# Optimization experiments

Measured on AMD Instinct MI355X. Metric: run time of the kernel, lower is better.

The kernel has to match this reference:

```python
import jax, jax.numpy as jnp
import numpy as np

INF = 10000.0
HEAD_SIZE = 64
HEADS = 12


def _rope_tables(seqlen, dim, dtype=jnp.float32):
    inv_freq = 1.0 / (10000.0 ** (jnp.arange(0, dim, 2, dtype=dtype) / dim))
    t = jnp.arange(seqlen, dtype=dtype)
    freqs = t[:, None] * inv_freq[None, :]  # [n, dim//2]
    return jnp.sin(freqs), jnp.cos(freqs)


def _apply_rope(t, sin, cos):
    # t: [b, n, d]; sin/cos: [n, d//2]
    t1, t2 = t[..., 0::2], t[..., 1::2]
    r1 = t1 * cos - t2 * sin
    r2 = t1 * sin + t2 * cos
    return jnp.stack([r1, r2], axis=-1).reshape(t.shape)


def setup_inputs() -> dict:
    key = jax.random.key(0)
    k1, k2, k3, k4, k5, k6 = jax.random.split(key, 6)
    B, N, H = 16, 512, 1024
    inputs = jax.random.normal(k1, (B, N, H), dtype=jnp.float32)
    attention_mask = jax.random.randint(k2, (B, N), 0, 2, dtype=jnp.int32)
    w1 = jax.random.normal(k3, (H, 2 * HEAD_SIZE), dtype=jnp.float32) * 0.02
    b1 = jax.random.normal(k4, (2 * HEAD_SIZE,), dtype=jnp.float32) * 0.02
    w2 = jax.random.normal(k5, (2 * HEAD_SIZE, 2 * HEADS), dtype=jnp.float32) * 0.02
    b2 = jax.random.normal(k6, (2 * HEADS,), dtype=jnp.float32) * 0.02
    return {"inputs": inputs, "attention_mask": attention_mask,
            "w1": w1, "b1": b1, "w2": w2, "b2": b2}


def reference(inputs, attention_mask, w1, b1, w2, b2):
    B, N, _ = inputs.shape
    x = inputs @ w1 + b1  # [b, n, 2*head_size]
    qw, kw = x[..., 0::2], x[..., 1::2]  # each [b, n, head_size]
    sin, cos = _rope_tables(N, HEAD_SIZE, x.dtype)
    qw = _apply_rope(qw, sin, cos)
    kw = _apply_rope(kw, sin, cos)
    logits = jnp.einsum('bmd,bnd->bmn', qw, kw) / (HEAD_SIZE ** 0.5)
    bias = jnp.swapaxes(x @ w2 + b2, 1, 2) / 2.0  # [b, 2*heads, n]
    logits = logits[:, None] + bias[:, 0::2, None, :] + bias[:, 1::2, :, None]  # [b, h, m, n]
    am = attention_mask.astype(logits.dtype)
    pad_mask = 1.0 - am[:, None, None, :] * am[:, None, :, None]
    logits = logits - pad_mask * INF
    idx = jnp.arange(N)
    tril = (idx[:, None] > idx[None, :]).astype(logits.dtype)  # strict lower triangle
    logits = logits - tril * INF
    return logits
```

## Files before the change

kernel.cpp:

```cpp
#include <hip/hip_runtime.h>

typedef __bf16 bf16_t;
typedef bf16_t bf16x4 __attribute__((ext_vector_type(4)));
typedef bf16_t bf16x8 __attribute__((ext_vector_type(8)));
typedef float f32x4 __attribute__((ext_vector_type(4)));

#define INFV 10000.0f

__global__ __launch_bounds__(256) void k0_transpose(const float* __restrict__ w1,
                                                    bf16_t* __restrict__ w1T) {
    __shared__ float s[32][36];
    const int t = threadIdx.x;
    const int k0 = (blockIdx.x & 31) * 32;
    const int c0 = (blockIdx.x >> 5) * 32;
    {
        const int r = t >> 3, cc = (t & 7) * 4;
        *(float4*)&s[r][cc] = *(const float4*)&w1[(size_t)(k0 + r) * 128 + c0 + cc];
    }
    __syncthreads();
    {
        const int cr = t >> 3, kk = (t & 7) * 4;
        bf16x4 v;
        v[0] = (bf16_t)s[kk + 0][cr];
        v[1] = (bf16_t)s[kk + 1][cr];
        v[2] = (bf16_t)s[kk + 2][cr];
        v[3] = (bf16_t)s[kk + 3][cr];
        *(bf16x4*)&w1T[(size_t)(c0 + cr) * 1024 + k0 + kk] = v;
    }
}

__global__ __launch_bounds__(512) void k1_proj(
    const float* __restrict__ inputs,
    const bf16_t* __restrict__ w1T,
    const float* __restrict__ b1,
    const float* __restrict__ w2,
    const float* __restrict__ b2,
    bf16_t* __restrict__ qg,
    bf16_t* __restrict__ kg,
    float* __restrict__ biasT)
{
    __shared__ bf16_t s_a[2][32][72];
    __shared__ float s_x[32][132];
    __shared__ float s_w2T[24][132];

    const int t = threadIdx.x;
    const int row0 = blockIdx.x * 32;
    const int lane = t & 63, wave = t >> 6;
    const int cn = lane & 15, kgrp = lane >> 4;
    const int rg = (wave & 1) * 16;
    const int cg = (wave >> 1) * 32;

    for (int i = t; i < 3072; i += 512) {
        int j = i / 24, c = i - j * 24;
        s_w2T[c][j] = w2[i];
    }

    const int sr = t >> 4;
    const int sc = (t & 15) * 4;
    const float* asrc = inputs + (size_t)(row0 + sr) * 1024 + sc;

    const bf16_t* bp0 = w1T + (size_t)(cg + 0 * 16 + cn) * 1024 + kgrp * 8;
    const bf16_t* bp1 = w1T + (size_t)(cg + 1 * 16 + cn) * 1024 + kgrp * 8;

    f32x4 acc[2][2] = {};
    float4 pfA[2];
    bf16x8 bfr[2][2][2];

    {
        float4 v = *(const float4*)(asrc);
        bf16x4 b;
        b[0] = (bf16_t)v.x; b[1] = (bf16_t)v.y; b[2] = (bf16_t)v.z; b[3] = (bf16_t)v.w;
        *(bf16x4*)&s_a[0][sr][sc] = b;
    }
    pfA[1] = *(const float4*)(asrc + 64);
    pfA[0] = *(const float4*)(asrc + 128);
    bfr[0][0][0] = *(const bf16x8*)(bp0 + 0);
    bfr[0][0][1] = *(const bf16x8*)(bp0 + 32);
    bfr[0][1][0] = *(const bf16x8*)(bp1 + 0);
    bfr[0][1][1] = *(const bf16x8*)(bp1 + 32);
    __syncthreads();

#pragma unroll
    for (int kt = 0; kt < 16; ++kt) {
        const int p = kt & 1;
        if (kt < 15) {
            const int o = (kt + 1) * 64;
            bfr[p ^ 1][0][0] = *(const bf16x8*)(bp0 + o);
            bfr[p ^ 1][0][1] = *(const bf16x8*)(bp0 + o + 32);
            bfr[p ^ 1][1][0] = *(const bf16x8*)(bp1 + o);
            bfr[p ^ 1][1][1] = *(const bf16x8*)(bp1 + o + 32);
        }
        {
            bf16x8 af0 = *(const bf16x8*)&s_a[p][rg + cn][kgrp * 8];
            bf16x8 af1 = *(const bf16x8*)&s_a[p][rg + cn][32 + kgrp * 8];
            acc[0][p] = __builtin_amdgcn_mfma_f32_16x16x32_bf16(af0, bfr[p][0][0], acc[0][p], 0, 0, 0);
            acc[0][p] = __builtin_amdgcn_mfma_f32_16x16x32_bf16(af1, bfr[p][0][1], acc[0][p], 0, 0, 0);
            acc[1][p] = __builtin_amdgcn_mfma_f32_16x16x32_bf16(af0, bfr[p][1][0], acc[1][p], 0, 0, 0);
            acc[1][p] = __builtin_amdgcn_mfma_f32_16x16x32_bf16(af1, bfr[p][1][1], acc[1][p], 0, 0, 0);
        }
        if (kt < 15) {
            float4 v = pfA[(kt + 1) & 1];
            bf16x4 b;
            b[0] = (bf16_t)v.x; b[1] = (bf16_t)v.y; b[2] = (bf16_t)v.z; b[3] = (bf16_t)v.w;
            *(bf16x4*)&s_a[p ^ 1][sr][sc] = b;
        }
        if (kt < 13) {
            pfA[(kt + 3) & 1] = *(const float4*)(asrc + (kt + 3) * 64);
        }
        __syncthreads();
    }

#pragma unroll
    for (int tt = 0; tt < 2; ++tt) {
        const int col = cg + tt * 16 + cn;
        const float bb = b1[col];
        f32x4 sum = acc[tt][0] + acc[tt][1];
#pragma unroll
        for (int r = 0; r < 4; ++r)
            s_x[rg + kgrp * 4 + r][col] = sum[r] + bb;
    }
    __syncthreads();

    {
        const int r = t >> 4;
        const int i0 = (t & 15) * 2;
        const int rowg = row0 + r;
        const int n = rowg & 511;
        bf16x4 qv, kv;
#pragma unroll
        for (int u = 0; u < 2; ++u) {
            const int i = i0 + u;
            float fr = (float)n * exp2f((float)i * -0.4152410118609203f);
            float sv, cv;
            sincosf(fr, &sv, &cv);
            float x0 = s_x[r][4 * i + 0];
            float x1 = s_x[r][4 * i + 1];
            float x2 = s_x[r][4 * i + 2];
            float x3 = s_x[r][4 * i + 3];
            qv[2 * u]     = (bf16_t)(x0 * cv - x2 * sv);
            qv[2 * u + 1] = (bf16_t)(x0 * sv + x2 * cv);
            kv[2 * u]     = (bf16_t)(x1 * cv - x3 * sv);
            kv[2 * u + 1] = (bf16_t)(x1 * sv + x3 * cv);
        }
        *(bf16x4*)&qg[(size_t)rowg * 64 + 2 * i0] = qv;
        *(bf16x4*)&kg[(size_t)rowg * 64 + 2 * i0] = kv;
    }

    {
        const int r = t >> 4;
        const int cb = t & 15;
        if (cb < 12) {
            const int c0 = cb * 2;
            float sum0 = 0.f, sum1 = 0.f;
#pragma unroll 4
            for (int j = 0; j < 128; j += 4) {
                float4 xv = *(const float4*)&s_x[r][j];
                float4 wa = *(const float4*)&s_w2T[c0 + 0][j];
                float4 wb = *(const float4*)&s_w2T[c0 + 1][j];
                sum0 += xv.x * wa.x + xv.y * wa.y + xv.z * wa.z + xv.w * wa.w;
                sum1 += xv.x * wb.x + xv.y * wb.y + xv.z * wb.z + xv.w * wb.w;
            }
            const int rowg = row0 + r;
            const int bb = rowg >> 9, n = rowg & 511;
            float* bp = biasT + (size_t)bb * 12288 + n;
            bp[(size_t)(c0 + 0) * 512] = (sum0 + b2[c0 + 0]) * 0.5f;
            bp[(size_t)(c0 + 1) * 512] = (sum1 + b2[c0 + 1]) * 0.5f;
        }
    }
}

__global__ __launch_bounds__(256) void k2_logits(
    const bf16_t* __restrict__ qg, const bf16_t* __restrict__ kg,
    const float* __restrict__ biasT, const int* __restrict__ am,
    float* __restrict__ out)
{
    __shared__ float s_be[12][64], s_bo[12][64];
    __shared__ float s_pm[64], s_pn[64];

    const int t = threadIdx.x;
    const int b = blockIdx.z;
    const int m0 = blockIdx.y * 64;
    const int n0 = blockIdx.x * 64;

    for (int i = t; i < 768; i += 256) {
        const int h = i >> 6, j = i & 63;
        s_be[h][j] = biasT[(size_t)b * 12288 + (size_t)(2 * h) * 512 + n0 + j];
        s_bo[h][j] = biasT[(size_t)b * 12288 + (size_t)(2 * h + 1) * 512 + m0 + j];
    }
    if (t < 64) s_pm[t] = (float)am[b * 512 + m0 + t];
    else if (t < 128) s_pn[t - 64] = (float)am[b * 512 + n0 + (t - 64)];

    const int lane = t & 63, wave = t >> 6;
    const int cn = lane & 15, kgrp = lane >> 4;

    const bf16_t* qp = qg + ((size_t)(b * 512 + m0 + wave * 16 + cn)) * 64 + kgrp * 8;
    bf16x8 qb0 = *(const bf16x8*)qp;
    bf16x8 qb1 = *(const bf16x8*)(qp + 32);

    f32x4 acc[4] = {};
#pragma unroll
    for (int nt = 0; nt < 4; ++nt) {
        const bf16_t* kp = kg + ((size_t)(b * 512 + n0 + nt * 16 + cn)) * 64 + kgrp * 8;
        bf16x8 ka0 = *(const bf16x8*)kp;
        bf16x8 ka1 = *(const bf16x8*)(kp + 32);
        acc[nt] = __builtin_amdgcn_mfma_f32_16x16x32_bf16(ka0, qb0, acc[nt], 0, 0, 0);
        acc[nt] = __builtin_amdgcn_mfma_f32_16x16x32_bf16(ka1, qb1, acc[nt], 0, 0, 0);
    }
    __syncthreads();

    const int rgrp = lane >> 4;
    const int m_loc = wave * 16 + cn;
    const int m = m0 + m_loc;
    const float am_m = s_pm[m_loc];

#pragma unroll
    for (int nt = 0; nt < 4; ++nt) {
#pragma unroll
        for (int r = 0; r < 4; ++r) {
            const int n_loc = nt * 16 + rgrp * 4 + r;
            float v = acc[nt][r] * 0.125f;
            v -= (1.0f - am_m * s_pn[n_loc]) * INFV;
            if (m > n0 + n_loc) v -= INFV;
            acc[nt][r] = v;
        }
    }

    float* ob = out + (size_t)b * 3145728 + (size_t)m * 512 + n0;
#pragma unroll
    for (int h = 0; h < 12; ++h) {
        const float bo = s_bo[h][m_loc];
        const f32x4 bov = {bo, bo, bo, bo};
#pragma unroll
        for (int nt = 0; nt < 4; ++nt) {
            const f32x4 be4 = *(const f32x4*)&s_be[h][nt * 16 + rgrp * 4];
            f32x4 w = acc[nt] + be4 + bov;
            *(f32x4*)&ob[(size_t)h * 262144 + nt * 16 + rgrp * 4] = w;
        }
    }
}

extern "C" void kernel_launch(void* const* d_in, const int* in_sizes, int n_in,
                              void* d_out, int out_size, void* d_ws, size_t ws_size,
                              hipStream_t stream) {
    const float* inputs = (const float*)d_in[0];
    const int*   am     = (const int*)d_in[1];
    const float* w1     = (const float*)d_in[2];
    const float* b1     = (const float*)d_in[3];
    const float* w2     = (const float*)d_in[4];
    const float* b2     = (const float*)d_in[5];
    float* out = (float*)d_out;

    bf16_t* w1T   = (bf16_t*)d_ws;
    bf16_t* qg    = w1T + 131072;
    bf16_t* kg    = qg + 524288;
    float*  biasT = (float*)(kg + 524288);

    k0_transpose<<<128, 256, 0, stream>>>(w1, w1T);
    k1_proj<<<256, 512, 0, stream>>>(inputs, w1T, b1, w2, b2, qg, kg, biasT);
    k2_logits<<<dim3(8, 8, 16), 256, 0, stream>>>(qg, kg, biasT, am, out);
}
```

Measured before the change: 67.16 us.

## Fuse projection and logits kernels with a global atomic grid barrier

Merges the projection kernel and the logits kernel into one persistent launch of 256 blocks. A global atomic counter acts as a grid-wide barrier once Q, K and the bias are written. After the barrier each 512-thread block splits into two 256-thread halves, and each half handles two 64x64 logits tiles. This removes one kernel launch and the gap between kernels, but relies on all 256 blocks being co-resident and adds a memset plus spin-waiting. The logits phase also runs with fewer resident blocks than the previous 1024-block grid, which may lower the overlap of memory traffic on the write-bound output.

```diff
diff --git a/kernel.cpp b/kernel.cpp
--- a/kernel.cpp
+++ b/kernel.cpp
@@ -29,212 +29,229 @@
     }
 }
 
-__global__ __launch_bounds__(512) void k1_proj(
+__global__ __launch_bounds__(512) void k12_fused(
     const float* __restrict__ inputs,
     const bf16_t* __restrict__ w1T,
     const float* __restrict__ b1,
     const float* __restrict__ w2,
     const float* __restrict__ b2,
+    const int* __restrict__ am,
     bf16_t* __restrict__ qg,
     bf16_t* __restrict__ kg,
-    float* __restrict__ biasT)
+    float* __restrict__ biasT,
+    float* __restrict__ out,
+    unsigned* __restrict__ ctr)
 {
     __shared__ bf16_t s_a[2][32][72];
     __shared__ float s_x[32][132];
     __shared__ float s_w2T[24][132];
+    __shared__ float s_be[2][12][64], s_bo[2][12][64];
+    __shared__ float s_pm[2][64], s_pn[2][64];
 
     const int t = threadIdx.x;
-    const int row0 = blockIdx.x * 32;
-    const int lane = t & 63, wave = t >> 6;
-    const int cn = lane & 15, kgrp = lane >> 4;
-    const int rg = (wave & 1) * 16;
-    const int cg = (wave >> 1) * 32;
-
-    for (int i = t; i < 3072; i += 512) {
-        int j = i / 24, c = i - j * 24;
-        s_w2T[c][j] = w2[i];
-    }
-
-    const int sr = t >> 4;
-    const int sc = (t & 15) * 4;
-    const float* asrc = inputs + (size_t)(row0 + sr) * 1024 + sc;
-
-    const bf16_t* bp0 = w1T + (size_t)(cg + 0 * 16 + cn) * 1024 + kgrp * 8;
-    const bf16_t* bp1 = w1T + (size_t)(cg + 1 * 16 + cn) * 1024 + kgrp * 8;
-
-    f32x4 acc[2][2] = {};
-    float4 pfA[2];
-    bf16x8 bfr[2][2][2];
-
-    {
-        float4 v = *(const float4*)(asrc);
-        bf16x4 b;
-        b[0] = (bf16_t)v.x; b[1] = (bf16_t)v.y; b[2] = (bf16_t)v.z; b[3] = (bf16_t)v.w;
-        *(bf16x4*)&s_a[0][sr][sc] = b;
-    }
-    pfA[1] = *(const float4*)(asrc + 64);
-    pfA[0] = *(const float4*)(asrc + 128);
-    bfr[0][0][0] = *(const bf16x8*)(bp0 + 0);
-    bfr[0][0][1] = *(const bf16x8*)(bp0 + 32);
-    bfr[0][1][0] = *(const bf16x8*)(bp1 + 0);
-    bfr[0][1][1] = *(const bf16x8*)(bp1 + 32);
-    __syncthreads();
-
-#pragma unroll
-    for (int kt = 0; kt < 16; ++kt) {
-        const int p = kt & 1;
-        if (kt < 15) {
-            const int o = (kt + 1) * 64;
-            bfr[p ^ 1][0][0] = *(const bf16x8*)(bp0 + o);
-            bfr[p ^ 1][0][1] = *(const bf16x8*)(bp0 + o + 32);
-            bfr[p ^ 1][1][0] = *(const bf16x8*)(bp1 + o);
-            bfr[p ^ 1][1][1] = *(const bf16x8*)(bp1 + o + 32);
-        }
+
+    {
+        const int row0 = blockIdx.x * 32;
+        const int lane = t & 63, wave = t >> 6;
+        const int cn = lane & 15, kgrp = lane >> 4;
+        const int rg = (wave & 1) * 16;
+        const int cg = (wave >> 1) * 32;
+
+        for (int i = t; i < 3072; i += 512) {
+            int j = i / 24, c = i - j * 24;
+            s_w2T[c][j] = w2[i];
+        }
+
+        const int sr = t >> 4;
+        const int sc = (t & 15) * 4;
+        const float* asrc = inputs + (size_t)(row0 + sr) * 1024 + sc;
+
+        const bf16_t* bp0 = w1T + (size_t)(cg + 0 * 16 + cn) * 1024 + kgrp * 8;
+        const bf16_t* bp1 = w1T + (size_t)(cg + 1 * 16 + cn) * 1024 + kgrp * 8;
+
+        f32x4 acc[2][2] = {};
+        float4 pfA[2];
+        bf16x8 bfr[2][2][2];
+
         {
-            bf16x8 af0 = *(const bf16x8*)&s_a[p][rg + cn][kgrp * 8];
-            bf16x8 af1 = *(const bf16x8*)&s_a[p][rg + cn][32 + kgrp * 8];
-            acc[0][p] = __builtin_amdgcn_mfma_f32_16x16x32_bf16(af0, bfr[p][0][0], acc[0][p], 0, 0, 0);
-            acc[0][p] = __builtin_amdgcn_mfma_f32_16x16x32_bf16(af1, bfr[p][0][1], acc[0][p], 0, 0, 0);
-            acc[1][p] = __builtin_amdgcn_mfma_f32_16x16x32_bf16(af0, bfr[p][1][0], acc[1][p], 0, 0, 0);
-            acc[1][p] = __builtin_amdgcn_mfma_f32_16x16x32_bf16(af1, bfr[p][1][1], acc[1][p], 0, 0, 0);
-        }
-        if (kt < 15) {
-            float4 v = pfA[(kt + 1) & 1];
+            float4 v = *(const float4*)(asrc);
             bf16x4 b;
             b[0] = (bf16_t)v.x; b[1] = (bf16_t)v.y; b[2] = (bf16_t)v.z; b[3] = (bf16_t)v.w;
-            *(bf16x4*)&s_a[p ^ 1][sr][sc] = b;
-        }
-        if (kt < 13) {
-            pfA[(kt + 3) & 1] = *(const float4*)(asrc + (kt + 3) * 64);
-        }
+            *(bf16x4*)&s_a[0][sr][sc] = b;
+        }
+        pfA[1] = *(const float4*)(asrc + 64);
+        pfA[0] = *(const float4*)(asrc + 128);
+        bfr[0][0][0] = *(const bf16x8*)(bp0 + 0);
+        bfr[0][0][1] = *(const bf16x8*)(bp0 + 32);
+        bfr[0][1][0] = *(const bf16x8*)(bp1 + 0);
+        bfr[0][1][1] = *(const bf16x8*)(bp1 + 32);
         __syncthreads();
-    }
-
-#pragma unroll
-    for (int tt = 0; tt < 2; ++tt) {
-        const int col = cg + tt * 16 + cn;
-        const float bb = b1[col];
-        f32x4 sum = acc[tt][0] + acc[tt][1];
-#pragma unroll
-        for (int r = 0; r < 4; ++r)
-            s_x[rg + kgrp * 4 + r][col] = sum[r] + bb;
-    }
+
+#pragma unroll
+        for (int kt = 0; kt < 16; ++kt) {
+            const int p = kt & 1;
+            if (kt < 15) {
+                const int o = (kt + 1) * 64;
+                bfr[p ^ 1][0][0] = *(const bf16x8*)(bp0 + o);
+                bfr[p ^ 1][0][1] = *(const bf16x8*)(bp0 + o + 32);
+                bfr[p ^ 1][1][0] = *(const bf16x8*)(bp1 + o);
+                bfr[p ^ 1][1][1] = *(const bf16x8*)(bp1 + o + 32);
+            }
+            {
+                bf16x8 af0 = *(const bf16x8*)&s_a[p][rg + cn][kgrp * 8];
+                bf16x8 af1 = *(const bf16x8*)&s_a[p][rg + cn][32 + kgrp * 8];
+                acc[0][p] = __builtin_amdgcn_mfma_f32_16x16x32_bf16(af0, bfr[p][0][0], acc[0][p], 0, 0, 0);
+                acc[0][p] = __builtin_amdgcn_mfma_f32_16x16x32_bf16(af1, bfr[p][0][1], acc[0][p], 0, 0, 0);
+                acc[1][p] = __builtin_amdgcn_mfma_f32_16x16x32_bf16(af0, bfr[p][1][0], acc[1][p], 0, 0, 0);
+                acc[1][p] = __builtin_amdgcn_mfma_f32_16x16x32_bf16(af1, bfr[p][1][1], acc[1][p], 0, 0, 0);
+            }
+            if (kt < 15) {
+                float4 v = pfA[(kt + 1) & 1];
+                bf16x4 b;
+                b[0] = (bf16_t)v.x; b[1] = (bf16_t)v.y; b[2] = (bf16_t)v.z; b[3] = (bf16_t)v.w;
+                *(bf16x4*)&s_a[p ^ 1][sr][sc] = b;
+            }
+            if (kt < 13) {
+                pfA[(kt + 3) & 1] = *(const float4*)(asrc + (kt + 3) * 64);
+            }
+            __syncthreads();
+        }
+
+#pragma unroll
+        for (int tt = 0; tt < 2; ++tt) {
+            const int col = cg + tt * 16 + cn;
+            const float bb = b1[col];
+            f32x4 sum = acc[tt][0] + acc[tt][1];
+#pragma unroll
+            for (int r = 0; r < 4; ++r)
+                s_x[rg + kgrp * 4 + r][col] = sum[r] + bb;
+        }
+        __syncthreads();
+
+        {
+            const int r = t >> 4;
+            const int i0 = (t & 15) * 2;
+            const int rowg = row0 + r;
+            const int n = rowg & 511;
+            bf16x4 qv, kv;
+#pragma unroll
+            for (int u = 0; u < 2; ++u) {
+                const int i = i0 + u;
+                float fr = (float)n * exp2f((float)i * -0.4152410118609203f);
+                float sv, cv;
+                sincosf(fr, &sv, &cv);
+                float x0 = s_x[r][4 * i + 0];
+                float x1 = s_x[r][4 * i + 1];
+                float x2 = s_x[r][4 * i + 2];
+                float x3 = s_x[r][4 * i + 3];
+                qv[2 * u]     = (bf16_t)(x0 * cv - x2 * sv);
+                qv[2 * u + 1] = (bf16_t)(x0 * sv + x2 * cv);
+                kv[2 * u]     = (bf16_t)(x1 * cv - x3 * sv);
+                kv[2 * u + 1] = (bf16_t)(x1 * sv + x3 * cv);
+            }
+            *(bf16x4*)&qg[(size_t)rowg * 64 + 2 * i0] = qv;
+            *(bf16x4*)&kg[(size_t)rowg * 64 + 2 * i0] = kv;
+        }
+
+        {
+            const int r = t >> 4;
+            const int cb = t & 15;
+            if (cb < 12) {
+                const int c0 = cb * 2;
+                float sum0 = 0.f, sum1 = 0.f;
+#pragma unroll 4
+                for (int j = 0; j < 128; j += 4) {
+                    float4 xv = *(const float4*)&s_x[r][j];
+                    float4 wa = *(const float4*)&s_w2T[c0 + 0][j];
+                    float4 wb = *(const float4*)&s_w2T[c0 + 1][j];
+                    sum0 += xv.x * wa.x + xv.y * wa.y + xv.z * wa.z + xv.w * wa.w;
+                    sum1 += xv.x * wb.x + xv.y * wb.y + xv.z * wb.z + xv.w * wb.w;
+                }
+                const int rowg = row0 + r;
+                const int bb = rowg >> 9, n = rowg & 511;
+                float* bp = biasT + (size_t)bb * 12288 + n;
+                bp[(size_t)(c0 + 0) * 512] = (sum0 + b2[c0 + 0]) * 0.5f;
+                bp[(size_t)(c0 + 1) * 512] = (sum1 + b2[c0 + 1]) * 0.5f;
+            }
+        }
+    }
+
     __syncthreads();
-
-    {
-        const int r = t >> 4;
-        const int i0 = (t & 15) * 2;
-        const int rowg = row0 + r;
-        const int n = rowg & 511;
-        bf16x4 qv, kv;
-#pragma unroll
-        for (int u = 0; u < 2; ++u) {
-            const int i = i0 + u;
-            float fr = (float)n * exp2f((float)i * -0.4152410118609203f);
-            float sv, cv;
-            sincosf(fr, &sv, &cv);
-            float x0 = s_x[r][4 * i + 0];
-            float x1 = s_x[r][4 * i + 1];
-            float x2 = s_x[r][4 * i + 2];
-            float x3 = s_x[r][4 * i + 3];
-            qv[2 * u]     = (bf16_t)(x0 * cv - x2 * sv);
-            qv[2 * u + 1] = (bf16_t)(x0 * sv + x2 * cv);
-            kv[2 * u]     = (bf16_t)(x1 * cv - x3 * sv);
-            kv[2 * u + 1] = (bf16_t)(x1 * sv + x3 * cv);
-        }
-        *(bf16x4*)&qg[(size_t)rowg * 64 + 2 * i0] = qv;
-        *(bf16x4*)&kg[(size_t)rowg * 64 + 2 * i0] = kv;
-    }
-
-    {
-        const int r = t >> 4;
-        const int cb = t & 15;
-        if (cb < 12) {
-            const int c0 = cb * 2;
-            float sum0 = 0.f, sum1 = 0.f;
-#pragma unroll 4
-            for (int j = 0; j < 128; j += 4) {
-                float4 xv = *(const float4*)&s_x[r][j];
-                float4 wa = *(const float4*)&s_w2T[c0 + 0][j];
-                float4 wb = *(const float4*)&s_w2T[c0 + 1][j];
-                sum0 += xv.x * wa.x + xv.y * wa.y + xv.z * wa.z + xv.w * wa.w;
-                sum1 += xv.x * wb.x + xv.y * wb.y + xv.z * wb.z + xv.w * wb.w;
-            }
-            const int rowg = row0 + r;
-            const int bb = rowg >> 9, n = rowg & 511;
-            float* bp = biasT + (size_t)bb * 12288 + n;
-            bp[(size_t)(c0 + 0) * 512] = (sum0 + b2[c0 + 0]) * 0.5f;
-            bp[(size_t)(c0 + 1) * 512] = (sum1 + b2[c0 + 1]) * 0.5f;
-        }
-    }
-}
-
-__global__ __launch_bounds__(256) void k2_logits(
-    const bf16_t* __restrict__ qg, const bf16_t* __restrict__ kg,
-    const float* __restrict__ biasT, const int* __restrict__ am,
-    float* __restrict__ out)
-{
-    __shared__ float s_be[12][64], s_bo[12][64];
-    __shared__ float s_pm[64], s_pn[64];
-
-    const int t = threadIdx.x;
-    const int b = blockIdx.z;
-    const int m0 = blockIdx.y * 64;
-    const int n0 = blockIdx.x * 64;
-
-    for (int i = t; i < 768; i += 256) {
-        const int h = i >> 6, j = i & 63;
-        s_be[h][j] = biasT[(size_t)b * 12288 + (size_t)(2 * h) * 512 + n0 + j];
-        s_bo[h][j] = biasT[(size_t)b * 12288 + (size_t)(2 * h + 1) * 512 + m0 + j];
-    }
-    if (t < 64) s_pm[t] = (float)am[b * 512 + m0 + t];
-    else if (t < 128) s_pn[t - 64] = (float)am[b * 512 + n0 + (t - 64)];
-
-    const int lane = t & 63, wave = t >> 6;
-    const int cn = lane & 15, kgrp = lane >> 4;
-
-    const bf16_t* qp = qg + ((size_t)(b * 512 + m0 + wave * 16 + cn)) * 64 + kgrp * 8;
-    bf16x8 qb0 = *(const bf16x8*)qp;
-    bf16x8 qb1 = *(const bf16x8*)(qp + 32);
-
-    f32x4 acc[4] = {};
-#pragma unroll
-    for (int nt = 0; nt < 4; ++nt) {
-        const bf16_t* kp = kg + ((size_t)(b * 512 + n0 + nt * 16 + cn)) * 64 + kgrp * 8;
-        bf16x8 ka0 = *(const bf16x8*)kp;
-        bf16x8 ka1 = *(const bf16x8*)(kp + 32);
-        acc[nt] = __builtin_amdgcn_mfma_f32_16x16x32_bf16(ka0, qb0, acc[nt], 0, 0, 0);
-        acc[nt] = __builtin_amdgcn_mfma_f32_16x16x32_bf16(ka1, qb1, acc[nt], 0, 0, 0);
+    if (t == 0) {
+        __threadfence();
+        atomicAdd(ctr, 1u);
+        while (atomicAdd(ctr, 0u) < 256u) __builtin_amdgcn_s_sleep(8);
     }
     __syncthreads();
-
-    const int rgrp = lane >> 4;
-    const int m_loc = wave * 16 + cn;
-    const int m = m0 + m_loc;
-    const float am_m = s_pm[m_loc];
-
-#pragma unroll
-    for (int nt = 0; nt < 4; ++nt) {
-#pragma unroll
-        for (int r = 0; r < 4; ++r) {
-            const int n_loc = nt * 16 + rgrp * 4 + r;
-            float v = acc[nt][r] * 0.125f;
-            v -= (1.0f - am_m * s_pn[n_loc]) * INFV;
-            if (m > n0 + n_loc) v -= INFV;
-            acc[nt][r] = v;
-        }
-    }
-
-    float* ob = out + (size_t)b * 3145728 + (size_t)m * 512 + n0;
-#pragma unroll
-    for (int h = 0; h < 12; ++h) {
-        const float bo = s_bo[h][m_loc];
-        const f32x4 bov = {bo, bo, bo, bo};
-#pragma unroll
-        for (int nt = 0; nt < 4; ++nt) {
-            const f32x4 be4 = *(const f32x4*)&s_be[h][nt * 16 + rgrp * 4];
-            f32x4 w = acc[nt] + be4 + bov;
-            *(f32x4*)&ob[(size_t)h * 262144 + nt * 16 + rgrp * 4] = w;
+    __threadfence();
+
+    {
+        const int h = t >> 8;
+        const int t2 = t & 255;
+
+#pragma unroll
+        for (int it = 0; it < 2; ++it) {
+            const int tid = blockIdx.x * 4 + it * 2 + h;
+            const int b = tid >> 6;
+            const int m0 = ((tid >> 3) & 7) * 64;
+            const int n0 = (tid & 7) * 64;
+
+            for (int i = t2; i < 768; i += 256) {
+                const int hh = i >> 6, j = i & 63;
+                s_be[h][hh][j] = biasT[(size_t)b * 12288 + (size_t)(2 * hh) * 512 + n0 + j];
+                s_bo[h][hh][j] = biasT[(size_t)b * 12288 + (size_t)(2 * hh + 1) * 512 + m0 + j];
+            }
+            if (t2 < 64) s_pm[h][t2] = (float)am[b * 512 + m0 + t2];
+            else if (t2 < 128) s_pn[h][t2 - 64] = (float)am[b * 512 + n0 + (t2 - 64)];
+            __syncthreads();
+
+            const int lane = t2 & 63, wave = t2 >> 6;
+            const int cn = lane & 15, kgrp = lane >> 4;
+
+            const bf16_t* qp = qg + ((size_t)(b * 512 + m0 + wave * 16 + cn)) * 64 + kgrp * 8;
+            bf16x8 qb0 = *(const bf16x8*)qp;
+            bf16x8 qb1 = *(const bf16x8*)(qp + 32);
+
+            f32x4 acc[4] = {};
+#pragma unroll
+            for (int nt = 0; nt < 4; ++nt) {
+                const bf16_t* kp = kg + ((size_t)(b * 512 + n0 + nt * 16 + cn)) * 64 + kgrp * 8;
+                bf16x8 ka0 = *(const bf16x8*)kp;
+                bf16x8 ka1 = *(const bf16x8*)(kp + 32);
+                acc[nt] = __builtin_amdgcn_mfma_f32_16x16x32_bf16(ka0, qb0, acc[nt], 0, 0, 0);
+                acc[nt] = __builtin_amdgcn_mfma_f32_16x16x32_bf16(ka1, qb1, acc[nt], 0, 0, 0);
+            }
+
+            const int rgrp = lane >> 4;
+            const int m_loc = wave * 16 + cn;
+            const int m = m0 + m_loc;
+            const float am_m = s_pm[h][m_loc];
+
+#pragma unroll
+            for (int nt = 0; nt < 4; ++nt) {
+#pragma unroll
+                for (int r = 0; r < 4; ++r) {
+                    const int n_loc = nt * 16 + rgrp * 4 + r;
+                    float v = acc[nt][r] * 0.125f;
+                    v -= (1.0f - am_m * s_pn[h][n_loc]) * INFV;
+                    if (m > n0 + n_loc) v -= INFV;
+                    acc[nt][r] = v;
+                }
+            }
+
+            float* ob = out + (size_t)b * 3145728 + (size_t)m * 512 + n0;
+#pragma unroll
+            for (int hh = 0; hh < 12; ++hh) {
+                const float bo = s_bo[h][hh][m_loc];
+                const f32x4 bov = {bo, bo, bo, bo};
+#pragma unroll
+                for (int nt = 0; nt < 4; ++nt) {
+                    const f32x4 be4 = *(const f32x4*)&s_be[h][hh][nt * 16 + rgrp * 4];
+                    f32x4 w = acc[nt] + be4 + bov;
+                    *(f32x4*)&ob[(size_t)hh * 262144 + nt * 16 + rgrp * 4] = w;
+                }
+            }
+            __syncthreads();
         }
     }
 }
@@ -254,8 +271,10 @@
     bf16_t* qg    = w1T + 131072;
     bf16_t* kg    = qg + 524288;
     float*  biasT = (float*)(kg + 524288);
-
+    unsigned* ctr = (unsigned*)((char*)d_ws + 3145728);
+
+    hipMemsetAsync(ctr, 0, 64, stream);
     k0_transpose<<<128, 256, 0, stream>>>(w1, w1T);
-    k1_proj<<<256, 512, 0, stream>>>(inputs, w1T, b1, w2, b2, qg, kg, biasT);
-    k2_logits<<<dim3(8, 8, 16), 256, 0, stream>>>(qg, kg, biasT, am, out);
+    k12_fused<<<256, 512, 0, stream>>>(inputs, w1T, b1, w2, b2, am,
+                                       qg, kg, biasT, out, ctr);
 }
```

Result: slower. 114.0 us (+69.7%).

## Restructure logits kernel to stage full K row and write coalesced output rows

Applied to the files above, without the earlier changes.

The logits kernel now gives each block a 32-row m-tile across all 512 n columns. The batch's K is staged in swizzled LDS and the QK tile is staged through shared memory. Each wave then writes contiguous 1KB output row segments instead of scattered 16-byte pieces. This targets output store coalescing on a write-bound kernel (about 100MB of output), at the cost of large LDS use (about 160KB) and fewer blocks (256), which limits occupancy.

```diff
diff --git a/kernel.cpp b/kernel.cpp
--- a/kernel.cpp
+++ b/kernel.cpp
@@ -169,73 +169,109 @@
     }
 }
 
-__global__ __launch_bounds__(256) void k2_logits(
+__global__ __launch_bounds__(512) void k2_logits(
     const bf16_t* __restrict__ qg, const bf16_t* __restrict__ kg,
     const float* __restrict__ biasT, const int* __restrict__ am,
     float* __restrict__ out)
 {
-    __shared__ float s_be[12][64], s_bo[12][64];
-    __shared__ float s_pm[64], s_pn[64];
+    __shared__ bf16_t s_k[512 * 64];
+    __shared__ float s_qk[32][516];
+    __shared__ float s_be[12][512];
+    __shared__ float s_bo[12][32];
+    __shared__ float s_pn[512];
+    __shared__ float s_pm[32];
 
     const int t = threadIdx.x;
-    const int b = blockIdx.z;
-    const int m0 = blockIdx.y * 64;
-    const int n0 = blockIdx.x * 64;
-
-    for (int i = t; i < 768; i += 256) {
-        const int h = i >> 6, j = i & 63;
-        s_be[h][j] = biasT[(size_t)b * 12288 + (size_t)(2 * h) * 512 + n0 + j];
-        s_bo[h][j] = biasT[(size_t)b * 12288 + (size_t)(2 * h + 1) * 512 + m0 + j];
-    }
-    if (t < 64) s_pm[t] = (float)am[b * 512 + m0 + t];
-    else if (t < 128) s_pn[t - 64] = (float)am[b * 512 + n0 + (t - 64)];
-
-    const int lane = t & 63, wave = t >> 6;
+    const int b = blockIdx.x >> 4;
+    const int m0 = (blockIdx.x & 15) * 32;
+    const int lane = t & 63, w = t >> 6;
     const int cn = lane & 15, kgrp = lane >> 4;
 
-    const bf16_t* qp = qg + ((size_t)(b * 512 + m0 + wave * 16 + cn)) * 64 + kgrp * 8;
-    bf16x8 qb0 = *(const bf16x8*)qp;
-    bf16x8 qb1 = *(const bf16x8*)(qp + 32);
-
-    f32x4 acc[4] = {};
+    bf16x8 qb[2][2];
+#pragma unroll
+    for (int mt = 0; mt < 2; ++mt) {
+        const bf16_t* qp = qg + ((size_t)(b * 512 + m0 + mt * 16 + cn)) * 64 + kgrp * 8;
+        qb[mt][0] = *(const bf16x8*)qp;
+        qb[mt][1] = *(const bf16x8*)(qp + 32);
+    }
+
+    {
+        const bf16_t* kb = kg + (size_t)b * 512 * 64;
+#pragma unroll
+        for (int i = 0; i < 8; ++i) {
+            const int id = i * 512 + t;
+            const int row = id >> 3, j = id & 7;
+            bf16x8 v = *(const bf16x8*)(kb + id * 8);
+            *(bf16x8*)((char*)s_k + row * 128 + ((j * 16) ^ ((row & 7) << 4))) = v;
+        }
+    }
+    for (int i = t; i < 6144; i += 512) {
+        const int h = i >> 9, n = i & 511;
+        s_be[h][n] = biasT[(size_t)b * 12288 + (size_t)(2 * h) * 512 + n];
+    }
+    if (t < 384) {
+        const int h = t >> 5, m = t & 31;
+        s_bo[h][m] = biasT[(size_t)b * 12288 + (size_t)(2 * h + 1) * 512 + m0 + m];
+    }
+    s_pn[t] = (float)am[b * 512 + t];
+    if (t < 32) s_pm[t] = (float)am[b * 512 + m0 + t];
+    __syncthreads();
+
+    f32x4 acc[2][4] = {};
 #pragma unroll
     for (int nt = 0; nt < 4; ++nt) {
-        const bf16_t* kp = kg + ((size_t)(b * 512 + n0 + nt * 16 + cn)) * 64 + kgrp * 8;
-        bf16x8 ka0 = *(const bf16x8*)kp;
-        bf16x8 ka1 = *(const bf16x8*)(kp + 32);
-        acc[nt] = __builtin_amdgcn_mfma_f32_16x16x32_bf16(ka0, qb0, acc[nt], 0, 0, 0);
-        acc[nt] = __builtin_amdgcn_mfma_f32_16x16x32_bf16(ka1, qb1, acc[nt], 0, 0, 0);
-    }
-    __syncthreads();
-
-    const int rgrp = lane >> 4;
-    const int m_loc = wave * 16 + cn;
-    const int m = m0 + m_loc;
-    const float am_m = s_pm[m_loc];
-
-#pragma unroll
-    for (int nt = 0; nt < 4; ++nt) {
-#pragma unroll
-        for (int r = 0; r < 4; ++r) {
-            const int n_loc = nt * 16 + rgrp * 4 + r;
-            float v = acc[nt][r] * 0.125f;
-            v -= (1.0f - am_m * s_pn[n_loc]) * INFV;
-            if (m > n0 + n_loc) v -= INFV;
-            acc[nt][r] = v;
-        }
-    }
-
-    float* ob = out + (size_t)b * 3145728 + (size_t)m * 512 + n0;
-#pragma unroll
-    for (int h = 0; h < 12; ++h) {
-        const float bo = s_bo[h][m_loc];
-        const f32x4 bov = {bo, bo, bo, bo};
-#pragma unroll
-        for (int nt = 0; nt < 4; ++nt) {
-            const f32x4 be4 = *(const f32x4*)&s_be[h][nt * 16 + rgrp * 4];
-            f32x4 w = acc[nt] + be4 + bov;
-            *(f32x4*)&ob[(size_t)h * 262144 + nt * 16 + rgrp * 4] = w;
-        }
+        const int n = w * 64 + nt * 16 + cn;
+        const char* krow = (const char*)s_k + n * 128;
+        const int sw = (n & 7) << 4;
+        bf16x8 ka0 = *(const bf16x8*)(krow + ((kgrp * 16) ^ sw));
+        bf16x8 ka1 = *(const bf16x8*)(krow + ((64 + kgrp * 16) ^ sw));
+#pragma unroll
+        for (int mt = 0; mt < 2; ++mt) {
+            acc[mt][nt] = __builtin_amdgcn_mfma_f32_16x16x32_bf16(ka0, qb[mt][0], acc[mt][nt], 0, 0, 0);
+            acc[mt][nt] = __builtin_amdgcn_mfma_f32_16x16x32_bf16(ka1, qb[mt][1], acc[mt][nt], 0, 0, 0);
+        }
+    }
+#pragma unroll
+    for (int mt = 0; mt < 2; ++mt)
+#pragma unroll
+        for (int nt = 0; nt < 4; ++nt)
+            *(f32x4*)&s_qk[mt * 16 + cn][w * 64 + nt * 16 + kgrp * 4] = acc[mt][nt];
+    __syncthreads();
+
+    {
+        const int m = t >> 4;
+        const int nb = (t & 15) * 32;
+        const float pmv = s_pm[m];
+        const int mg = m0 + m;
+#pragma unroll
+        for (int u = 0; u < 8; ++u) {
+            const int n = nb + u * 4;
+            f32x4 v = *(f32x4*)&s_qk[m][n];
+#pragma unroll
+            for (int r = 0; r < 4; ++r) {
+                float x = v[r] * 0.125f;
+                x -= (1.0f - pmv * s_pn[n + r]) * INFV;
+                if (mg > n + r) x -= INFV;
+                v[r] = x;
+            }
+            *(f32x4*)&s_qk[m][n] = v;
+        }
+    }
+    __syncthreads();
+
+    float* ob = out + (size_t)b * 3145728 + (size_t)m0 * 512;
+#pragma unroll 4
+    for (int jb = 0; jb < 96; ++jb) {
+        const int job = jb * 8 + w;
+        const int h = job >> 6;
+        const int rem = job & 63;
+        const int m = rem >> 1;
+        const int n = (rem & 1) * 256 + lane * 4;
+        const f32x4 v = *(const f32x4*)&s_qk[m][n];
+        const f32x4 be4 = *(const f32x4*)&s_be[h][n];
+        const float bo = s_bo[h][m];
+        const f32x4 o = v + be4 + (f32x4){bo, bo, bo, bo};
+        *(f32x4*)&ob[(size_t)h * 262144 + (size_t)m * 512 + n] = o;
     }
 }
 
@@ -257,5 +293,5 @@
 
     k0_transpose<<<128, 256, 0, stream>>>(w1, w1T);
     k1_proj<<<256, 512, 0, stream>>>(inputs, w1T, b1, w2, b2, qg, kg, biasT);
-    k2_logits<<<dim3(8, 8, 16), 256, 0, stream>>>(qg, kg, biasT, am, out);
-}
+    k2_logits<<<256, 512, 0, stream>>>(qg, kg, biasT, am, out);
+}
```

New measurement: 70.73 us. 1.05x slower.
